# Kernel optimization log

Hardware: AMD Instinct MI355X
Metric: run time of the kernel (lower is better)

Reference implementation:

```python
import jax, jax.numpy as jnp
import numpy as np
from jax import lax

D_MODEL, D_INNER, D_STATE, D_CONV, DT_RANK = 128, 256, 16, 4, 8
BATCH, SEQ = 8, 4096


def setup_inputs() -> dict:
    key = jax.random.key(0)
    ks = jax.random.split(key, 13)
    g = lambda k, shape, fan: (jax.random.normal(k, shape, jnp.float32) / np.sqrt(fan)).astype(jnp.float32)
    inp = {
        "s": jax.random.normal(ks[0], (BATCH, SEQ, D_MODEL), jnp.float32),
        "in_proj_w": g(ks[1], (2 * D_INNER, D_MODEL), D_MODEL),
        "conv_w": g(ks[2], (D_INNER, 1, D_CONV), D_CONV),
        "conv_b": jnp.zeros((D_INNER,), jnp.float32),
        "x_proj_w": g(ks[3], (DT_RANK + 2 * D_STATE, D_INNER), D_INNER),
        "dt_proj_w": g(ks[4], (D_INNER, DT_RANK), DT_RANK),
        "dt_proj_b": jax.random.uniform(ks[5], (D_INNER,), jnp.float32, -4.0, -2.0),  # softplus(b) small, like mamba dt init
        "A_log": jnp.log(jnp.broadcast_to(jnp.arange(1, D_STATE + 1, dtype=jnp.float32), (D_INNER, D_STATE))),
        "D_skip": jnp.ones((D_INNER,), jnp.float32),
        "out_proj_w": g(ks[6], (D_MODEL, D_INNER), D_INNER),
        "ln_gamma": jnp.ones((D_MODEL,), jnp.float32),
        "ln_beta": jnp.zeros((D_MODEL,), jnp.float32),
        "fc_w": g(ks[7], (D_MODEL, D_MODEL), D_MODEL),
    }
    return inp


def _mamba(s, in_proj_w, conv_w, conv_b, x_proj_w, dt_proj_w, dt_proj_b, A_log, D_skip, out_proj_w):
    B, L, _ = s.shape
    xz = jnp.einsum("bld,ed->ble", s, in_proj_w)           # [B,L,2*D_INNER]
    x, z = jnp.split(xz, 2, axis=-1)                        # each [B,L,D_INNER]
    # causal depthwise conv1d
    xc = jnp.transpose(x, (0, 2, 1))                        # [B,D_INNER,L]
    xc = jnp.pad(xc, ((0, 0), (0, 0), (D_CONV - 1, 0)))
    xc = lax.conv_general_dilated(xc, conv_w, (1,), "VALID",
                                  dimension_numbers=("NCH", "OIH", "NCH"),
                                  feature_group_count=D_INNER)
    x = jax.nn.silu(jnp.transpose(xc + conv_b[None, :, None], (0, 2, 1)))  # [B,L,D_INNER]
    # input-dependent dt, B, C
    x_dbl = jnp.einsum("bld,ed->ble", x, x_proj_w)
    dt = x_dbl[..., :DT_RANK]
    Bc = x_dbl[..., DT_RANK:DT_RANK + D_STATE]              # [B,L,D_STATE]
    Cc = x_dbl[..., DT_RANK + D_STATE:]                     # [B,L,D_STATE]
    dt = jax.nn.softplus(jnp.einsum("blr,dr->bld", dt, dt_proj_w) + dt_proj_b)  # [B,L,D_INNER]
    A = -jnp.exp(A_log)                                     # [D_INNER,D_STATE]

    def step(h, inp):
        dt_t, b_t, c_t, u_t = inp                           # [B,Di],[B,Ds],[B,Ds],[B,Di]
        dA = jnp.exp(dt_t[:, :, None] * A)                  # [B,Di,Ds]
        dBu = (dt_t * u_t)[:, :, None] * b_t[:, None, :]
        h = dA * h + dBu
        y = jnp.einsum("bds,bs->bd", h, c_t)
        return h, y

    h0 = jnp.zeros((B, D_INNER, D_STATE), x.dtype)
    xs = (jnp.swapaxes(dt, 0, 1), jnp.swapaxes(Bc, 0, 1), jnp.swapaxes(Cc, 0, 1), jnp.swapaxes(x, 0, 1))
    _, ys = lax.scan(step, h0, xs)                          # ys: [L,B,D_INNER]
    y = jnp.swapaxes(ys, 0, 1) + x * D_skip
    y = y * jax.nn.silu(z)
    return jnp.einsum("bld,od->blo", y, out_proj_w)         # [B,L,D_MODEL]


def reference(s, in_proj_w, conv_w, conv_b, x_proj_w, dt_proj_w, dt_proj_b, A_log, D_skip, out_proj_w, ln_gamma, ln_beta, fc_w):
    h = _mamba(s, in_proj_w, conv_w, conv_b, x_proj_w, dt_proj_w, dt_proj_b, A_log, D_skip, out_proj_w)
    mu = jnp.mean(h, axis=-1, keepdims=True)
    var = jnp.mean(jnp.square(h - mu), axis=-1, keepdims=True)
    hn = (h - mu) * lax.rsqrt(var + 1e-5) * ln_gamma + ln_beta
    return jax.nn.relu(jnp.einsum("bld,od->blo", hn, fc_w))
```

## Files before the change

### kernel.cpp

```cpp
#include <hip/hip_runtime.h>
#include <math.h>

#define B_ 8
#define L_ 4096
#define DM 128
#define DI 256
#define DSN 16
#define RK 8
#define M_ (B_*L_)
#define NC 128
#define CH 32
#define CH2 64

typedef __attribute__((ext_vector_type(8))) short bfrag;
typedef __attribute__((ext_vector_type(4))) float ffrag;
typedef __attribute__((ext_vector_type(2))) float f32x2;

__device__ __forceinline__ float silu_f(float x) {
  return x * __builtin_amdgcn_rcpf(1.f + __expf(-x));
}
__device__ __forceinline__ float softplus_f(float x) {
  return (x > 20.f) ? x : __logf(1.f + __expf(x));
}

__device__ __forceinline__ unsigned short f2bf(float f) {
  unsigned int u = __builtin_bit_cast(unsigned int, f);
  unsigned int r = (u + 0x7FFFu + ((u >> 16) & 1u)) >> 16;
  return (unsigned short)r;
}
__device__ __forceinline__ unsigned int f2bf2(float lo, float hi) {
  return (unsigned int)f2bf(lo) | ((unsigned int)f2bf(hi) << 16);
}
__device__ __forceinline__ float bf2f(unsigned int us) {
  return __builtin_bit_cast(float, us << 16);
}

__global__ __launch_bounds__(256)
void prep_weights(const float* __restrict__ w_in, const float* __restrict__ xw,
                  const float* __restrict__ ow, const float* __restrict__ fcw,
                  unsigned short* __restrict__ w_in_b, unsigned short* __restrict__ xw_b,
                  unsigned short* __restrict__ ow_b, unsigned short* __restrict__ fcw_b) {
  const int i = blockIdx.x * 256 + threadIdx.x;
  const float* src; unsigned short* dst; int j;
  if (i < 16384)      { src = w_in; dst = w_in_b; j = i; }
  else if (i < 18944) { src = xw;   dst = xw_b;   j = i - 16384; }
  else if (i < 27136) { src = ow;   dst = ow_b;   j = i - 18944; }
  else if (i < 31232) { src = fcw;  dst = fcw_b;  j = i - 27136; }
  else return;
  float4 v = *(const float4*)&src[j << 2];
  uint2 p = {f2bf2(v.x, v.y), f2bf2(v.z, v.w)};
  *(uint2*)&dst[j << 2] = p;
}

__global__ __launch_bounds__(256, 4)
void xproj_dtproj(const float* __restrict__ s, const unsigned short* __restrict__ w_in_b,
                  const unsigned short* __restrict__ xw_b,
                  const float* __restrict__ dtw, const float* __restrict__ dtpb,
                  const float* __restrict__ cw, const float* __restrict__ cb,
                  const float* __restrict__ alog,
                  float* __restrict__ Bb, float* __restrict__ Cb,
                  unsigned int* __restrict__ udt,
                  unsigned short* __restrict__ zsb,
                  unsigned short* __restrict__ cP, unsigned short* __restrict__ cHe) {
  __shared__ __align__(16) char pool[38960];
  unsigned short* As = (unsigned short*)pool;
  unsigned short* ua = (unsigned short*)pool;
  unsigned short* hx = (unsigned short*)(pool + 16896);
  float* dtr_s = (float*)(pool + 35376);
  float* Bs_l  = (float*)(pool + 36912);
  const int t = threadIdx.x;
  const int p0 = blockIdx.x << 5;
  const int w = t >> 6, l = t & 63, q = l >> 4, col = l & 15;

  for (int i = t; i < 48 * 32; i += 256) {
    int row = i >> 5, c4 = i & 31;
    int pos = (row < 32) ? (p0 + row) : (p0 - 16 + (row - 32));
    if (pos < 0) pos = 0;
    float4 av = *(const float4*)&s[pos * 128 + (c4 << 2)];
    uint2 ap = {f2bf2(av.x, av.y), f2bf2(av.z, av.w)};
    *(uint2*)&As[row * 136 + (c4 << 2)] = ap;
  }
  __syncthreads();
  for (int jt = 0; jt < 8; ++jt) {
    const int wrow0 = jt << 6;
    const int T = (jt < 4) ? 12 : 8;
    for (int tile = w; tile < T; tile += 4) {
      const int mt = tile >> 2, nt = tile & 3;
      ffrag acc = {0.f, 0.f, 0.f, 0.f};
#pragma unroll
      for (int s8 = 0; s8 < 4; ++s8) {
        int k0 = s8 * 32 + q * 8;
        bfrag af = *(const bfrag*)&As[((mt << 4) + col) * 136 + k0];
        bfrag wf = *(const bfrag*)&w_in_b[(wrow0 + (nt << 4) + col) * 128 + k0];
        acc = __builtin_amdgcn_mfma_f32_16x16x32_bf16(wf, af, acc, 0, 0, 0);
      }
      const int chb = (nt << 4) + (q << 2);
      if (jt < 4) {
        uint2 pk = {f2bf2(acc[0], acc[1]), f2bf2(acc[2], acc[3])};
        const int ch = (jt << 6) + chb;
        if (mt < 2) {
          *(uint2*)&hx[(3 + (mt << 4) + col) * 264 + ch] = pk;
        } else if (col >= 13) {
          *(uint2*)&hx[(col - 13) * 264 + ch] = pk;
        }
      } else {
        uint2 pk = {f2bf2(silu_f(acc[0]), silu_f(acc[1])),
                    f2bf2(silu_f(acc[2]), silu_f(acc[3]))};
        const int m = p0 + (mt << 4) + col;
        *(uint2*)&zsb[m * 256 + ((jt - 4) << 6) + chb] = pk;
      }
    }
  }
  __syncthreads();
  {
    const int k = t;
    const int lb = p0 & (L_ - 1);
    const float w0 = cw[k*4], w1 = cw[k*4+1], w2 = cw[k*4+2], w3 = cw[k*4+3];
    const float bias = cb[k];
    float x0 = (lb >= 3) ? bf2f((unsigned int)hx[0 * 264 + k]) : 0.f;
    float x1 = (lb >= 2) ? bf2f((unsigned int)hx[1 * 264 + k]) : 0.f;
    float x2 = (lb >= 1) ? bf2f((unsigned int)hx[2 * 264 + k]) : 0.f;
#pragma unroll 8
    for (int it = 0; it < 32; ++it) {
      float x3 = bf2f((unsigned int)hx[(3 + it) * 264 + k]);
      float u = silu_f(fmaf(w0, x0, fmaf(w1, x1, fmaf(w2, x2, fmaf(w3, x3, bias)))));
      ua[it * 264 + k] = f2bf(u);
      x0 = x1; x1 = x2; x2 = x3;
    }
  }
  __syncthreads();
  for (int tile = w; tile < 6; tile += 4) {
    const int mt = tile & 1, nt = tile >> 1;
    ffrag acc = {0.f, 0.f, 0.f, 0.f};
#pragma unroll
    for (int s8 = 0; s8 < 8; ++s8) {
      int k0 = s8 * 32 + q * 8;
      bfrag af = *(const bfrag*)&ua[((mt << 4) + col) * 264 + k0];
      const int nrow = (nt << 4) + col;
      bfrag wf = {0, 0, 0, 0, 0, 0, 0, 0};
      if (nrow < 40) wf = *(const bfrag*)&xw_b[nrow * 256 + k0];
      acc = __builtin_amdgcn_mfma_f32_16x16x32_bf16(wf, af, acc, 0, 0, 0);
    }
    const int ml = (mt << 4) + col;
    const int m = p0 + ml;
    const int n0 = (nt << 4) + (q << 2);
    float4 v = {acc[0], acc[1], acc[2], acc[3]};
    if (n0 < 8) {
      *(float4*)&dtr_s[ml * 12 + n0] = v;
    } else if (n0 < 24) {
      *(float4*)&Bb[m * 16 + (n0 - 8)] = v;
      *(float4*)&Bs_l[ml * 16 + (n0 - 8)] = v;
    } else if (n0 < 40) {
      *(float4*)&Cb[m * 16 + (n0 - 24)] = v;
    }
  }
  __syncthreads();
  {
    const int d = t;
    const int bb = p0 >> 12;
    const int cc = (p0 & (L_ - 1)) >> 5;
    const int bc = bb * NC + cc;
    float w8[8];
    *(float4*)&w8[0] = *(const float4*)&dtw[d * 8];
    *(float4*)&w8[4] = *(const float4*)&dtw[d * 8 + 4];
    const float bias = dtpb[d];
    float a[16];
    bool okl = true;
#pragma unroll
    for (int j = 0; j < 16; ++j) {
      a[j] = -__expf(alog[d * 16 + j]);
      float tgt = (float)(j + 1);
      okl = okl && (fabsf(a[j] + tgt) <= 1e-3f * tgt);
    }
    const bool fast = (bool)__all((int)okl);
    f32x2 h2[8] = {{0.f,0.f},{0.f,0.f},{0.f,0.f},{0.f,0.f},
                   {0.f,0.f},{0.f,0.f},{0.f,0.f},{0.f,0.f}};
    float sdt = 0.f;
#pragma unroll 2
    for (int pp = 0; pp < 32; ++pp) {
      float r0[8];
      *(float4*)&r0[0] = *(const float4*)&dtr_s[pp * 12];
      *(float4*)&r0[4] = *(const float4*)&dtr_s[pp * 12 + 4];
      float a2 = bias;
#pragma unroll
      for (int r2 = 0; r2 < 8; ++r2) a2 = fmaf(r0[r2], w8[r2], a2);
      float sp = softplus_f(a2);
      unsigned int uq = (unsigned int)ua[pp * 264 + d];
      unsigned short spb = f2bf(sp);
      udt[(p0 + pp) * 256 + d] = uq | ((unsigned int)spb << 16);
      float dtv = bf2f((unsigned int)spb);
      float uv  = bf2f(uq);
      float du = dtv * uv;
      sdt += dtv;
      const float* brow = &Bs_l[pp * 16];
      float4 b0 = *(const float4*)&brow[0];
      float4 b1 = *(const float4*)&brow[4];
      float4 b2 = *(const float4*)&brow[8];
      float4 b3 = *(const float4*)&brow[12];
      f32x2 B2[8] = {{b0.x,b0.y},{b0.z,b0.w},{b1.x,b1.y},{b1.z,b1.w},
                     {b2.x,b2.y},{b2.z,b2.w},{b3.x,b3.y},{b3.z,b3.w}};
      f32x2 du2 = {du, du};
      if (fast) {
        float e1 = __expf(-dtv);
        float e2 = e1 * e1;
        f32x2 dA = {e1, e2};
        f32x2 e22 = {e2, e2};
#pragma unroll
        for (int jj = 0; jj < 8; ++jj) {
          h2[jj] = dA * h2[jj] + du2 * B2[jj];
          dA = dA * e22;
        }
      } else {
#pragma unroll
        for (int j = 0; j < 16; ++j) {
          float dA = __expf(dtv * a[j]);
          h2[j >> 1][j & 1] = fmaf(dA, h2[j >> 1][j & 1], du * B2[j >> 1][j & 1]);
        }
      }
    }
#pragma unroll
    for (int j = 0; j < 16; ++j) {
      int o = (bc * 16 + j) * 256 + d;
      cP[o]  = f2bf(__expf(a[j] * sdt));
      cHe[o] = f2bf(h2[j >> 1][j & 1]);
    }
  }
}

__global__ __launch_bounds__(512)
void scan_combine(unsigned short* __restrict__ cP, const unsigned short* __restrict__ cHe) {
  __shared__ float segP[64 * 9], segH[64 * 9], segS[64 * 9];
  const int t = threadIdx.x;
  const int sdl = t & 63, seg = t >> 6;
  const int blk = blockIdx.x;
  const int b = blk >> 6, grp = blk & 63;
  const int sd = (grp << 6) + sdl;
  const int base = b * NC * 4096 + sd;
  float Pacc = 1.f, Hacc = 0.f;
#pragma unroll
  for (int i = 0; i < 16; ++i) {
    int idx = base + (seg * 16 + i) * 4096;
    float p = bf2f((unsigned int)cP[idx]);
    float he = bf2f((unsigned int)cHe[idx]);
    Hacc = fmaf(p, Hacc, he);
    Pacc *= p;
  }
  segP[sdl * 9 + seg] = Pacc;
  segH[sdl * 9 + seg] = Hacc;
  __syncthreads();
  if (t < 64) {
    float hs = 0.f;
#pragma unroll
    for (int s2 = 0; s2 < 8; ++s2) {
      segS[t * 9 + s2] = hs;
      hs = fmaf(segP[t * 9 + s2], hs, segH[t * 9 + s2]);
    }
  }
  __syncthreads();
  float hs = segS[sdl * 9 + seg];
#pragma unroll
  for (int i = 0; i < 16; ++i) {
    int idx = base + (seg * 16 + i) * 4096;
    float p = bf2f((unsigned int)cP[idx]);
    float he = bf2f((unsigned int)cHe[idx]);
    cP[idx] = f2bf(hs);
    hs = fmaf(p, hs, he);
  }
}

__global__ __launch_bounds__(512, 4)
void scan3_out_ln_fc(const unsigned int* __restrict__ udt,
                     const float* __restrict__ Bb, const float* __restrict__ Cb,
                     const float* __restrict__ alog, const unsigned short* __restrict__ hst,
                     const float* __restrict__ dsk,
                     const unsigned short* __restrict__ zsb,
                     const unsigned short* __restrict__ ow_b,
                     const float* __restrict__ gamma, const float* __restrict__ beta,
                     const unsigned short* __restrict__ fcw_b, float* __restrict__ out) {
  __shared__ float Bs[CH2 * 16];
  __shared__ float Cs[CH2 * 16];
  __shared__ unsigned short smA[64 * 264];
  const int bc = blockIdx.x;
  const int b = bc >> 6, cc = bc & 63;
  const int t = threadIdx.x;
  const int l = t & 63, w = t >> 6;
  const int chh = t >> 8;
  const int d = t & 255;
  const int base = b * L_ + (cc << 1) * CH;
  const int cbase = base + chh * CH;
  const int hc = b * NC + (cc << 1) + chh;
  if (t < CH2 * 4)           ((float4*)Bs)[t]            = *(const float4*)&Bb[base * 16 + (t << 2)];
  else if (t < CH2 * 8)      ((float4*)Cs)[t - CH2 * 4]  = *(const float4*)&Cb[base * 16 + ((t - CH2 * 4) << 2)];
  float a[16];
  bool okl = true;
#pragma unroll
  for (int j = 0; j < 16; ++j) {
    a[j] = -__expf(alog[d * 16 + j]);
    float tgt = (float)(j + 1);
    okl = okl && (fabsf(a[j] + tgt) <= 1e-3f * tgt);
  }
  const bool fast = (bool)__all((int)okl);
  const float dskv = dsk[d];
  f32x2 h2[8];
#pragma unroll
  for (int jj = 0; jj < 8; ++jj) {
    h2[jj][0] = bf2f((unsigned int)hst[(hc * 16 + (jj << 1)) * 256 + d]);
    h2[jj][1] = bf2f((unsigned int)hst[(hc * 16 + (jj << 1) + 1) * 256 + d]);
  }
  unsigned int wv0 = udt[cbase * 256 + d];
  unsigned int wv1 = udt[(cbase + 1) * 256 + d];
  unsigned short zv0 = zsb[cbase * 256 + d];
  unsigned short zv1 = zsb[(cbase + 1) * 256 + d];
  __syncthreads();
#pragma unroll 2
  for (int ll = 0; ll < CH; ++ll) {
    const int l2 = (ll + 2 < CH) ? ll + 2 : CH - 1;
    unsigned int wv2 = udt[(cbase + l2) * 256 + d];
    unsigned short zv2 = zsb[(cbase + l2) * 256 + d];
    const float* brow = &Bs[(chh * CH + ll) * 16];
    const float* crow = &Cs[(chh * CH + ll) * 16];
    float4 b0 = *(const float4*)&brow[0];
    float4 b1 = *(const float4*)&brow[4];
    float4 b2 = *(const float4*)&brow[8];
    float4 b3 = *(const float4*)&brow[12];
    float4 c0 = *(const float4*)&crow[0];
    float4 c1 = *(const float4*)&crow[4];
    float4 c2 = *(const float4*)&crow[8];
    float4 c3 = *(const float4*)&crow[12];
    float uv  = bf2f(wv0 & 0xFFFFu);
    float dtv = bf2f(wv0 >> 16);
    f32x2 B2[8] = {{b0.x,b0.y},{b0.z,b0.w},{b1.x,b1.y},{b1.z,b1.w},
                   {b2.x,b2.y},{b2.z,b2.w},{b3.x,b3.y},{b3.z,b3.w}};
    f32x2 C2[8] = {{c0.x,c0.y},{c0.z,c0.w},{c1.x,c1.y},{c1.z,c1.w},
                   {c2.x,c2.y},{c2.z,c2.w},{c3.x,c3.y},{c3.z,c3.w}};
    float du = dtv * uv;
    f32x2 du2 = {du, du};
    f32x2 y2 = {0.f, 0.f};
    if (fast) {
      float e1 = __expf(-dtv);
      float e2 = e1 * e1;
      f32x2 dA = {e1, e2};
      f32x2 e22 = {e2, e2};
#pragma unroll
      for (int jj = 0; jj < 8; ++jj) {
        h2[jj] = dA * h2[jj] + du2 * B2[jj];
        y2 = y2 + h2[jj] * C2[jj];
        dA = dA * e22;
      }
    } else {
#pragma unroll
      for (int j = 0; j < 16; ++j) {
        float dA = __expf(dtv * a[j]);
        float hh = fmaf(dA, h2[j >> 1][j & 1], du * B2[j >> 1][j & 1]);
        h2[j >> 1][j & 1] = hh;
        y2[j & 1] = fmaf(hh, C2[j >> 1][j & 1], y2[j & 1]);
      }
    }
    float y = y2.x + y2.y;
    float zs = bf2f((unsigned int)zv0);
    smA[(chh * CH + ll) * 264 + d] = f2bf(fmaf(uv, dskv, y) * zs);
    wv0 = wv1; wv1 = wv2; zv0 = zv1; zv1 = zv2;
  }
  const int q = l >> 4, col = l & 15;
  ffrag acc[2][4];
  float mu[4], rs[4];
  __syncthreads();
  if (t < 256) {
#pragma unroll
    for (int nt2 = 0; nt2 < 2; ++nt2)
#pragma unroll
      for (int nt = 0; nt < 4; ++nt) acc[nt2][nt] = (ffrag){0.f, 0.f, 0.f, 0.f};
#pragma unroll
    for (int s8 = 0; s8 < 8; ++s8) {
      int k0 = s8 * 32 + q * 8;
      bfrag af = *(const bfrag*)&smA[((w << 4) + col) * 264 + k0];
#pragma unroll
      for (int nt2 = 0; nt2 < 2; ++nt2)
#pragma unroll
        for (int nt = 0; nt < 4; ++nt) {
          bfrag wf = *(const bfrag*)&ow_b[((nt2 << 6) + (nt << 4) + col) * 256 + k0];
          acc[nt2][nt] = __builtin_amdgcn_mfma_f32_16x16x32_bf16(af, wf, acc[nt2][nt], 0, 0, 0);
        }
    }
#pragma unroll
    for (int i = 0; i < 4; ++i) {
      float s1 = 0.f, s2 = 0.f;
#pragma unroll
      for (int nt2 = 0; nt2 < 2; ++nt2)
#pragma unroll
        for (int nt = 0; nt < 4; ++nt) {
          float v = acc[nt2][nt][i];
          s1 += v; s2 = fmaf(v, v, s2);
        }
      s1 += __shfl_xor(s1, 1); s2 += __shfl_xor(s2, 1);
      s1 += __shfl_xor(s1, 2); s2 += __shfl_xor(s2, 2);
      s1 += __shfl_xor(s1, 4); s2 += __shfl_xor(s2, 4);
      s1 += __shfl_xor(s1, 8); s2 += __shfl_xor(s2, 8);
      mu[i] = s1 * (1.f / DM);
      float var = s2 * (1.f / DM) - mu[i] * mu[i];
      rs[i] = rsqrtf(var + 1e-5f);
    }
  }
  __syncthreads();
  if (t < 256) {
#pragma unroll
    for (int nt2 = 0; nt2 < 2; ++nt2)
#pragma unroll
      for (int nt = 0; nt < 4; ++nt) {
        int n = (nt2 << 6) + (nt << 4) + col;
        float g = gamma[n], be = beta[n];
#pragma unroll
        for (int i = 0; i < 4; ++i) {
          int r = (w << 4) + (q << 2) + i;
          smA[r * 136 + n] = f2bf(fmaf((acc[nt2][nt][i] - mu[i]) * rs[i], g, be));
        }
      }
  }
  __syncthreads();
  if (t < 256) {
    ffrag a2[8] = {{0.f,0.f,0.f,0.f},{0.f,0.f,0.f,0.f},{0.f,0.f,0.f,0.f},{0.f,0.f,0.f,0.f},
                   {0.f,0.f,0.f,0.f},{0.f,0.f,0.f,0.f},{0.f,0.f,0.f,0.f},{0.f,0.f,0.f,0.f}};
#pragma unroll
    for (int s8 = 0; s8 < 4; ++s8) {
      int k0 = s8 * 32 + q * 8;
      bfrag af = *(const bfrag*)&smA[((w << 4) + col) * 136 + k0];
#pragma unroll
      for (int nt = 0; nt < 8; ++nt) {
        bfrag wf = *(const bfrag*)&fcw_b[((nt << 4) + col) * 128 + k0];
        a2[nt] = __builtin_amdgcn_mfma_f32_16x16x32_bf16(af, wf, a2[nt], 0, 0, 0);
      }
    }
#pragma unroll
    for (int nt = 0; nt < 8; ++nt)
#pragma unroll
      for (int i = 0; i < 4; ++i) {
        int ml = (w << 4) + (q << 2) + i;
        out[(base + ml) * 128 + (nt << 4) + col] = fmaxf(a2[nt][i], 0.f);
      }
  }
}

extern "C" void kernel_launch(void* const* d_in, const int* in_sizes, int n_in,
                              void* d_out, int out_size, void* d_ws, size_t ws_size,
                              hipStream_t stream) {
  (void)in_sizes; (void)n_in; (void)out_size; (void)ws_size;
  const float* s    = (const float*)d_in[0];
  const float* w_in = (const float*)d_in[1];
  const float* cw   = (const float*)d_in[2];
  const float* cb   = (const float*)d_in[3];
  const float* xw   = (const float*)d_in[4];
  const float* dtw  = (const float*)d_in[5];
  const float* dtpb = (const float*)d_in[6];
  const float* alog = (const float*)d_in[7];
  const float* dsk  = (const float*)d_in[8];
  const float* ow   = (const float*)d_in[9];
  const float* gam  = (const float*)d_in[10];
  const float* bet  = (const float*)d_in[11];
  const float* fcw  = (const float*)d_in[12];
  float* out = (float*)d_out;
  float* ws  = (float*)d_ws;

  unsigned short* zsb  = (unsigned short*)(ws + 4194304);
  unsigned int*   udt  = (unsigned int*)(ws + 8388608);
  float*          Bb   = ws + 16777216;
  float*          Cb   = ws + 17301504;
  unsigned short* cP   = (unsigned short*)(ws + 17825792);
  unsigned short* cHe  = (unsigned short*)(ws + 19922944);
  unsigned short* w_in_b = (unsigned short*)(ws + 22020096);
  unsigned short* xw_b   = (unsigned short*)(ws + 22052864);
  unsigned short* ow_b   = (unsigned short*)(ws + 22057984);
  unsigned short* fcw_b  = (unsigned short*)(ws + 22074368);

  prep_weights<<<122, 256, 0, stream>>>(w_in, xw, ow, fcw, w_in_b, xw_b, ow_b, fcw_b);
  xproj_dtproj<<<M_ / CH, 256, 0, stream>>>(s, w_in_b, xw_b, dtw, dtpb, cw, cb, alog,
                                            Bb, Cb, udt, zsb, cP, cHe);
  scan_combine<<<512, 512, 0, stream>>>(cP, cHe);
  scan3_out_ln_fc<<<B_ * NC / 2, 512, 0, stream>>>(udt, Bb, Cb, alog, cP, dsk, zsb,
                                                   ow_b, gam, bet, fcw_b, out);
}
```

Baseline: 177.1 us.

## Spread out_proj/LN/fc epilogue across all eight waves with LDS-staged weights

The fused epilogue of the scan kernel now uses all 512 threads instead of only the first 256. Waves are split into four row groups and two column halves, so the LayerNorm statistics are combined across waves through small shared arrays. The out_proj and fc weight tiles are first copied into a new shared buffer, so MFMA operands come from LDS rather than repeated global loads. The extra buffer adds about 35KB of LDS per block and several barriers, which may cut the number of resident blocks per CU.

```diff
diff --git a/kernel.cpp b/kernel.cpp
--- a/kernel.cpp
+++ b/kernel.cpp
@@ -280,6 +280,8 @@
   __shared__ float Bs[CH2 * 16];
   __shared__ float Cs[CH2 * 16];
   __shared__ unsigned short smA[64 * 264];
+  __shared__ unsigned short smB[128 * 136];
+  __shared__ float pS1[128], pS2[128];
   const int bc = blockIdx.x;
   const int b = bc >> 6, cc = bc & 63;
   const int t = threadIdx.x;
@@ -362,82 +364,99 @@
     wv0 = wv1; wv1 = wv2; zv0 = zv1; zv1 = zv2;
   }
   const int q = l >> 4, col = l & 15;
-  ffrag acc[2][4];
-  float mu[4], rs[4];
-  __syncthreads();
-  if (t < 256) {
-#pragma unroll
-    for (int nt2 = 0; nt2 < 2; ++nt2)
-#pragma unroll
-      for (int nt = 0; nt < 4; ++nt) acc[nt2][nt] = (ffrag){0.f, 0.f, 0.f, 0.f};
+  const int rw = w & 3, np = w >> 2;
+  ffrag acc[2][2];
+  for (int nt2 = 0; nt2 < 2; ++nt2) {
+    __syncthreads();
+    for (int i = t; i < 64 * 32; i += 512) {
+      int row = i >> 5, c8 = (i & 31) << 3;
+      *(uint4*)&smB[row * 264 + c8] = *(const uint4*)&ow_b[((nt2 << 6) + row) * 256 + c8];
+    }
+    __syncthreads();
+#pragma unroll
+    for (int nt = 0; nt < 2; ++nt) acc[nt2][nt] = (ffrag){0.f, 0.f, 0.f, 0.f};
 #pragma unroll
     for (int s8 = 0; s8 < 8; ++s8) {
       int k0 = s8 * 32 + q * 8;
-      bfrag af = *(const bfrag*)&smA[((w << 4) + col) * 264 + k0];
-#pragma unroll
-      for (int nt2 = 0; nt2 < 2; ++nt2)
-#pragma unroll
-        for (int nt = 0; nt < 4; ++nt) {
-          bfrag wf = *(const bfrag*)&ow_b[((nt2 << 6) + (nt << 4) + col) * 256 + k0];
-          acc[nt2][nt] = __builtin_amdgcn_mfma_f32_16x16x32_bf16(af, wf, acc[nt2][nt], 0, 0, 0);
-        }
-    }
+      bfrag af = *(const bfrag*)&smA[((rw << 4) + col) * 264 + k0];
+#pragma unroll
+      for (int nt = 0; nt < 2; ++nt) {
+        bfrag bf_ = *(const bfrag*)&smB[((((np << 1) + nt) << 4) + col) * 264 + k0];
+        acc[nt2][nt] = __builtin_amdgcn_mfma_f32_16x16x32_bf16(af, bf_, acc[nt2][nt], 0, 0, 0);
+      }
+    }
+  }
+  float s1v[4], s2v[4];
+#pragma unroll
+  for (int i = 0; i < 4; ++i) {
+    float s1 = 0.f, s2 = 0.f;
+#pragma unroll
+    for (int nt2 = 0; nt2 < 2; ++nt2)
+#pragma unroll
+      for (int nt = 0; nt < 2; ++nt) {
+        float v = acc[nt2][nt][i];
+        s1 += v; s2 = fmaf(v, v, s2);
+      }
+    s1 += __shfl_xor(s1, 1); s2 += __shfl_xor(s2, 1);
+    s1 += __shfl_xor(s1, 2); s2 += __shfl_xor(s2, 2);
+    s1 += __shfl_xor(s1, 4); s2 += __shfl_xor(s2, 4);
+    s1 += __shfl_xor(s1, 8); s2 += __shfl_xor(s2, 8);
+    s1v[i] = s1; s2v[i] = s2;
+  }
+  if (col == 0) {
 #pragma unroll
     for (int i = 0; i < 4; ++i) {
-      float s1 = 0.f, s2 = 0.f;
-#pragma unroll
-      for (int nt2 = 0; nt2 < 2; ++nt2)
-#pragma unroll
-        for (int nt = 0; nt < 4; ++nt) {
-          float v = acc[nt2][nt][i];
-          s1 += v; s2 = fmaf(v, v, s2);
-        }
-      s1 += __shfl_xor(s1, 1); s2 += __shfl_xor(s2, 1);
-      s1 += __shfl_xor(s1, 2); s2 += __shfl_xor(s2, 2);
-      s1 += __shfl_xor(s1, 4); s2 += __shfl_xor(s2, 4);
-      s1 += __shfl_xor(s1, 8); s2 += __shfl_xor(s2, 8);
-      mu[i] = s1 * (1.f / DM);
-      float var = s2 * (1.f / DM) - mu[i] * mu[i];
-      rs[i] = rsqrtf(var + 1e-5f);
-    }
-  }
-  __syncthreads();
-  if (t < 256) {
-#pragma unroll
-    for (int nt2 = 0; nt2 < 2; ++nt2)
-#pragma unroll
-      for (int nt = 0; nt < 4; ++nt) {
-        int n = (nt2 << 6) + (nt << 4) + col;
-        float g = gamma[n], be = beta[n];
-#pragma unroll
-        for (int i = 0; i < 4; ++i) {
-          int r = (w << 4) + (q << 2) + i;
-          smA[r * 136 + n] = f2bf(fmaf((acc[nt2][nt][i] - mu[i]) * rs[i], g, be));
-        }
-      }
-  }
-  __syncthreads();
-  if (t < 256) {
-    ffrag a2[8] = {{0.f,0.f,0.f,0.f},{0.f,0.f,0.f,0.f},{0.f,0.f,0.f,0.f},{0.f,0.f,0.f,0.f},
-                   {0.f,0.f,0.f,0.f},{0.f,0.f,0.f,0.f},{0.f,0.f,0.f,0.f},{0.f,0.f,0.f,0.f}};
-#pragma unroll
-    for (int s8 = 0; s8 < 4; ++s8) {
-      int k0 = s8 * 32 + q * 8;
-      bfrag af = *(const bfrag*)&smA[((w << 4) + col) * 136 + k0];
-#pragma unroll
-      for (int nt = 0; nt < 8; ++nt) {
-        bfrag wf = *(const bfrag*)&fcw_b[((nt << 4) + col) * 128 + k0];
-        a2[nt] = __builtin_amdgcn_mfma_f32_16x16x32_bf16(af, wf, a2[nt], 0, 0, 0);
-      }
-    }
-#pragma unroll
-    for (int nt = 0; nt < 8; ++nt)
+      int r = (rw << 4) + (q << 2) + i;
+      pS1[(np << 6) + r] = s1v[i];
+      pS2[(np << 6) + r] = s2v[i];
+    }
+  }
+  __syncthreads();
+  float mu[4], rs[4];
+#pragma unroll
+  for (int i = 0; i < 4; ++i) {
+    int r = (rw << 4) + (q << 2) + i;
+    float s1 = pS1[r] + pS1[64 + r];
+    float s2 = pS2[r] + pS2[64 + r];
+    mu[i] = s1 * (1.f / DM);
+    float var = s2 * (1.f / DM) - mu[i] * mu[i];
+    rs[i] = rsqrtf(var + 1e-5f);
+  }
+#pragma unroll
+  for (int nt2 = 0; nt2 < 2; ++nt2)
+#pragma unroll
+    for (int nt = 0; nt < 2; ++nt) {
+      int n = (nt2 << 6) + ((((np << 1) + nt)) << 4) + col;
+      float g = gamma[n], be = beta[n];
 #pragma unroll
       for (int i = 0; i < 4; ++i) {
-        int ml = (w << 4) + (q << 2) + i;
-        out[(base + ml) * 128 + (nt << 4) + col] = fmaxf(a2[nt][i], 0.f);
-      }
-  }
+        int r = (rw << 4) + (q << 2) + i;
+        smA[r * 136 + n] = f2bf(fmaf((acc[nt2][nt][i] - mu[i]) * rs[i], g, be));
+      }
+    }
+  for (int i = t; i < 128 * 16; i += 512) {
+    int row = i >> 4, c8 = (i & 15) << 3;
+    *(uint4*)&smB[row * 136 + c8] = *(const uint4*)&fcw_b[row * 128 + c8];
+  }
+  __syncthreads();
+  ffrag a2[4] = {{0.f,0.f,0.f,0.f},{0.f,0.f,0.f,0.f},{0.f,0.f,0.f,0.f},{0.f,0.f,0.f,0.f}};
+#pragma unroll
+  for (int s8 = 0; s8 < 4; ++s8) {
+    int k0 = s8 * 32 + q * 8;
+    bfrag af = *(const bfrag*)&smA[((rw << 4) + col) * 136 + k0];
+#pragma unroll
+    for (int nt = 0; nt < 4; ++nt) {
+      bfrag bf_ = *(const bfrag*)&smB[((((np << 2) + nt) << 4) + col) * 136 + k0];
+      a2[nt] = __builtin_amdgcn_mfma_f32_16x16x32_bf16(af, bf_, a2[nt], 0, 0, 0);
+    }
+  }
+#pragma unroll
+  for (int nt = 0; nt < 4; ++nt)
+#pragma unroll
+    for (int i = 0; i < 4; ++i) {
+      int ml = (rw << 4) + (q << 2) + i;
+      out[(base + ml) * 128 + (((np << 2) + nt) << 4) + col] = fmaxf(a2[nt][i], 0.f);
+    }
 }
 
 extern "C" void kernel_launch(void* const* d_in, const int* in_sizes, int n_in,
```

Measured after the change: 167.0 us, median of 2. 1.06x faster.
